# Kernel tuning notes

Hardware: AMD Instinct MI355X
Metric: run time of the kernel (lower is better)

## Reference

```python
import jax, jax.numpy as jnp
import numpy as np

IN_DIM = 128
SLOT_SIZE = 64
NUM_SLOTS = 8
NUM_ITERS = 3
MLP_HDIM = 128
EPSILON = 1e-08


def _layernorm(x, g, b, eps=1e-5):
    m = jnp.mean(x, axis=-1, keepdims=True)
    v = jnp.mean((x - m) ** 2, axis=-1, keepdims=True)
    return (x - m) * jax.lax.rsqrt(v + eps) * g + b


def setup_inputs() -> dict:
    key = jax.random.key(0)
    ks = jax.random.split(key, 16)
    H, D, K, M = SLOT_SIZE, IN_DIM, NUM_SLOTS, MLP_HDIM
    x = jax.random.normal(ks[0], (32, 4096, D), dtype=jnp.float32)
    noise = jax.random.normal(ks[1], (32, K, H), dtype=jnp.float32)
    s = lambda k, shape, fan_in: jax.random.normal(k, shape, jnp.float32) * (1.0 / np.sqrt(fan_in))
    return {
        'x': x,
        'noise': noise,
        'Wq': s(ks[2], (H, H), H),            # project_q (no bias)
        'Wk': s(ks[3], (H, D), D),            # project_k
        'Wv': s(ks[4], (H, D), D),            # project_v
        'ln_in_g': jnp.ones((D,), jnp.float32), 'ln_in_b': jnp.zeros((D,), jnp.float32),
        'ln_sl_g': jnp.ones((H,), jnp.float32), 'ln_sl_b': jnp.zeros((H,), jnp.float32),
        'ln_mlp_g': jnp.ones((H,), jnp.float32), 'ln_mlp_b': jnp.zeros((H,), jnp.float32),
        'gru_w_ih': s(ks[5], (3 * H, H), H),  # PyTorch GRUCell weight_ih (r,z,n)
        'gru_w_hh': s(ks[6], (3 * H, H), H),
        'gru_b_ih': jnp.zeros((3 * H,), jnp.float32),
        'gru_b_hh': jnp.zeros((3 * H,), jnp.float32),
        'mlp_w1': s(ks[7], (M, H), H), 'mlp_b1': jnp.zeros((M,), jnp.float32),
        'mlp_w2': s(ks[8], (H, M), M), 'mlp_b2': jnp.zeros((H,), jnp.float32),
        'slots_mu': jnp.tile(jnp.linspace(-1.0, 1.0, K, dtype=jnp.float32)[None, :, None], (1, 1, H)),
        'slots_logsigma': jnp.full((1, K, H), -1.0, dtype=jnp.float32),
    }


def reference(x, noise, Wq, Wk, Wv, ln_in_g, ln_in_b, ln_sl_g, ln_sl_b,
              ln_mlp_g, ln_mlp_b, gru_w_ih, gru_w_hh, gru_b_ih, gru_b_hh,
              mlp_w1, mlp_b1, mlp_w2, mlp_b2, slots_mu, slots_logsigma):
    B = x.shape[0]
    H, K = SLOT_SIZE, NUM_SLOTS
    xn = _layernorm(x, ln_in_g, ln_in_b)
    k = jnp.einsum('bnd,hd->bnh', xn, Wk)  # [B,N,H]
    v = jnp.einsum('bnd,hd->bnh', xn, Wv)

    scale = jax.nn.softplus(slots_logsigma) + 1e-05
    slots = slots_mu + scale * noise  # rsample, broadcast over batch -> [B,K,H]

    def step(slots):
        slots_prev = slots
        s = _layernorm(slots, ln_sl_g, ln_sl_b)
        q = jnp.einsum('bkh,gh->bkg', s, Wq)  # [B,K,H]
        scores = (H ** -0.5) * jnp.einsum('bnh,bkh->bnk', k, q)
        attn = jax.nn.softmax(scores, axis=-1) + EPSILON  # softmax over slots
        attn = attn / jnp.sum(attn, axis=1, keepdims=True)  # normalize over inputs
        updates = jnp.einsum('bnk,bnh->bkh', attn, v)
        # PyTorch GRUCell: gates ordered (r, z, n)
        u = updates.reshape(-1, H)
        h = slots_prev.reshape(-1, H)
        gx = u @ gru_w_ih.T + gru_b_ih
        gh = h @ gru_w_hh.T + gru_b_hh
        xr, xz, xn_ = jnp.split(gx, 3, axis=-1)
        hr, hz, hn = jnp.split(gh, 3, axis=-1)
        r = jax.nn.sigmoid(xr + hr)
        z = jax.nn.sigmoid(xz + hz)
        n = jnp.tanh(xn_ + r * hn)
        slots = ((1.0 - z) * n + z * h).reshape(B, K, H)
        slots = _layernorm(slots, ln_mlp_g, ln_mlp_b)
        mlp_out = jax.nn.relu(slots @ mlp_w1.T + mlp_b1) @ mlp_w2.T + mlp_b2
        return slots + mlp_out

    for _ in range(NUM_ITERS):
        slots = step(slots)
    return slots
```

## Files before the change

### kernel.cpp

```cpp
#include <hip/hip_runtime.h>

typedef __attribute__((ext_vector_type(8))) short s16x8;
typedef __attribute__((ext_vector_type(4))) float f32x4;

#define DEV static __device__ __forceinline__

DEV float b2f(unsigned short u){
  unsigned int i = ((unsigned int)u) << 16;
  float f; __builtin_memcpy(&f, &i, 4); return f;
}
DEV unsigned short f2b(float f){
  unsigned int i; __builtin_memcpy(&i, &f, 4);
  i = i + 0x7fffu + ((i >> 16) & 1u);
  return (unsigned short)(i >> 16);
}
DEV f32x4 mfma16(s16x8 a, s16x8 b, f32x4 c){
  return __builtin_amdgcn_mfma_f32_16x16x32_bf16(a, b, c, 0, 0, 0);
}
DEV s16x8 ld8f(const float* p){
  const float4* q4 = (const float4*)p;
  float4 a = q4[0], b = q4[1];
  s16x8 r;
  r[0]=(short)f2b(a.x); r[1]=(short)f2b(a.y); r[2]=(short)f2b(a.z); r[3]=(short)f2b(a.w);
  r[4]=(short)f2b(b.x); r[5]=(short)f2b(b.y); r[6]=(short)f2b(b.z); r[7]=(short)f2b(b.w);
  return r;
}

template<int C> DEV float dpp_addstep(float x){
  int y = __builtin_amdgcn_update_dpp(0, __builtin_bit_cast(int, x), C, 0xF, 0xF, true);
  return x + __builtin_bit_cast(float, y);
}
DEV float rsum16(float v){
  v = dpp_addstep<0xB1>(v);
  v = dpp_addstep<0x4E>(v);
  v = dpp_addstep<0x141>(v);
  v = dpp_addstep<0x140>(v);
  return v;
}

__global__ __launch_bounds__(256) void k_wpack(
    const float* __restrict__ Wk, const float* __restrict__ Wv,
    const float* __restrict__ wih, const float* __restrict__ whh,
    const float* __restrict__ w1, const float* __restrict__ w2,
    const float* __restrict__ Wq,
    unsigned short* __restrict__ wkb, unsigned short* __restrict__ wvb,
    unsigned short* __restrict__ wall)
{
  int t = blockIdx.x * 256 + threadIdx.x;
  int off = t * 4;
  const float* src; unsigned short* dst;
  if      (off <  8192){ src = Wk  + off;         dst = wkb  + off; }
  else if (off < 16384){ src = Wv  + off -  8192; dst = wvb  + off - 8192; }
  else if (off < 28672){ src = wih + off - 16384; dst = wall + off - 16384; }
  else if (off < 40960){ src = whh + off - 28672; dst = wall + off - 16384; }
  else if (off < 49152){ src = w1  + off - 40960; dst = wall + off - 16384; }
  else if (off < 57344){ src = w2  + off - 49152; dst = wall + off - 16384; }
  else                 { src = Wq  + off - 57344; dst = wall + off - 16384; }
  float4 v = *(const float4*)src;
  ushort4 o;
  o.x = f2b(v.x); o.y = f2b(v.y); o.z = f2b(v.z); o.w = f2b(v.w);
  *(ushort4*)dst = o;
}

__global__ __launch_bounds__(256, 4) void k_lnkv7(
    const float* __restrict__ x,
    const unsigned short* __restrict__ wkb,
    const unsigned short* __restrict__ wvb,
    const float* __restrict__ lg,
    const float* __restrict__ lb,
    unsigned short* __restrict__ kg,
    unsigned short* __restrict__ vt,
    const float* __restrict__ noise,
    const float* __restrict__ mu,
    const float* __restrict__ lsg,
    const float* __restrict__ gsl,
    const float* __restrict__ bsl,
    const float* __restrict__ Wq,
    float* __restrict__ slots,
    unsigned short* __restrict__ qws)
{
  __shared__ __align__(16) unsigned int xs[128 * 68];
  const int tid = threadIdx.x;
  const int w = tid >> 6, ln = tid & 63;
  const int m16 = ln & 15, q = ln >> 4;

  if (blockIdx.x >= 1024){
    unsigned short* st = (unsigned short*)xs;
    float (*redS)[4] = (float(*)[4])((char*)xs + 2304);
    float (*redQ)[4] = (float(*)[4])((char*)xs + 2560);
    const int bi = blockIdx.x - 1024;
    const int r0 = bi * 16;
    const int cw = w*16 + m16;

    float sl[4], s1[4], s2[4];
    #pragma unroll
    for (int rr = 0; rr < 4; ++rr){
      int row = r0 + q*4 + rr;
      int k = row & 7;
      float v = mu[k*64 + cw] + (log1pf(expf(lsg[k*64 + cw])) + 1e-5f) * noise[row*64 + cw];
      sl[rr] = v;
      slots[row*64 + cw] = v;
      s1[rr] = rsum16(v);
      s2[rr] = rsum16(v*v);
    }
    if (m16 == 0){
      #pragma unroll
      for (int rr = 0; rr < 4; ++rr){ redS[q*4+rr][w] = s1[rr]; redQ[q*4+rr][w] = s2[rr]; }
    }
    __syncthreads();
    {
      const float gs = gsl[cw], bs = bsl[cw];
      #pragma unroll
      for (int rr = 0; rr < 4; ++rr){
        f32x4 aS = *(const f32x4*)redS[q*4+rr];
        f32x4 aQ = *(const f32x4*)redQ[q*4+rr];
        float tS = aS[0]+aS[1]+aS[2]+aS[3];
        float tQ = aQ[0]+aQ[1]+aQ[2]+aQ[3];
        float mean = tS*(1.f/64.f);
        float var  = tQ*(1.f/64.f) - mean*mean;
        float rs = rsqrtf(var + 1e-5f);
        float sq = (sl[rr] - mean)*rs*gs + bs;
        st[(q*4+rr)*72 + cw] = f2b(sq);
      }
    }
    __syncthreads();
    {
      f32x4 acc = {0,0,0,0};
      #pragma unroll
      for (int ks = 0; ks < 2; ++ks){
        s16x8 a = *(const s16x8*)(st + m16*72 + ks*32 + q*8);
        acc = mfma16(a, ld8f(Wq + cw*64 + ks*32 + q*8), acc);
      }
      #pragma unroll
      for (int rr = 0; rr < 4; ++rr){
        int row = r0 + q*4 + rr;
        int bb_ = row >> 3, kk = row & 7;
        qws[(bb_*16 + kk)*64 + cw] = f2b(acc[rr] * 0.125f);
      }
      int b0 = bi * 2;
      ((unsigned int*)(qws + (b0*16 + 8)*64))[tid] = 0u;
      ((unsigned int*)(qws + ((b0+1)*16 + 8)*64))[tid] = 0u;
    }
    return;
  }

  const int b = blockIdx.x >> 5;
  const int nbase = (blockIdx.x & 31) << 7;
  const long rowg0 = (long)b * 4096 + nbase;

  {
    const int c = m16;
    const float4 gA = *(const float4*)(lg + c*4);
    const float4 gB = *(const float4*)(lg + 64 + c*4);
    const float4 bA = *(const float4*)(lb + c*4);
    const float4 bB = *(const float4*)(lb + 64 + c*4);
    const float* base = x + (rowg0 + w*32 + q)*128;

    float4 va[4], vb[4];
    #pragma unroll
    for (int i = 0; i < 3; ++i){
      va[i] = *(const float4*)(base + i*512 + c*4);
      vb[i] = *(const float4*)(base + i*512 + 64 + c*4);
    }
    #pragma unroll
    for (int p = 0; p < 8; ++p){
      const int cur = p & 3;
      if (p < 5){
        const int nxt = (p+3) & 3;
        va[nxt] = *(const float4*)(base + (p+3)*512 + c*4);
        vb[nxt] = *(const float4*)(base + (p+3)*512 + 64 + c*4);
      }
      float4 u = va[cur], t = vb[cur];
      float s1 = (u.x + u.y) + (u.z + u.w) + (t.x + t.y) + (t.z + t.w);
      float s2 = (u.x*u.x + u.y*u.y) + (u.z*u.z + u.w*u.w)
               + (t.x*t.x + t.y*t.y) + (t.z*t.z + t.w*t.w);
      s1 = rsum16(s1);
      s2 = rsum16(s2);
      float mean = s1 * (1.f/128.f);
      float var  = s2 * (1.f/128.f) - mean*mean;
      float rs = rsqrtf(var + 1e-5f);
      float y0 = (u.x - mean)*rs*gA.x + bA.x;
      float y1 = (u.y - mean)*rs*gA.y + bA.y;
      float y2 = (u.z - mean)*rs*gA.z + bA.z;
      float y3 = (u.w - mean)*rs*gA.w + bA.w;
      float y4 = (t.x - mean)*rs*gB.x + bB.x;
      float y5 = (t.y - mean)*rs*gB.y + bB.y;
      float y6 = (t.z - mean)*rs*gB.z + bB.z;
      float y7 = (t.w - mean)*rs*gB.w + bB.w;
      uint2 pkA, pkB;
      pkA.x = (unsigned int)f2b(y0) | ((unsigned int)f2b(y1) << 16);
      pkA.y = (unsigned int)f2b(y2) | ((unsigned int)f2b(y3) << 16);
      pkB.x = (unsigned int)f2b(y4) | ((unsigned int)f2b(y5) << 16);
      pkB.y = (unsigned int)f2b(y6) | ((unsigned int)f2b(y7) << 16);
      const int r = w*32 + p*4 + q;
      *(uint2*)&xs[r*68 + c*2] = pkA;
      *(uint2*)&xs[r*68 + 32 + c*2] = pkB;
    }
  }

  s16x8 bw[4][4];
  #pragma unroll
  for (int t = 0; t < 4; ++t)
    #pragma unroll
    for (int kb = 0; kb < 4; ++kb)
      bw[kb][t] = *(const s16x8*)(wkb + (t*16 + m16)*128 + kb*32 + q*8);

  __syncthreads();

  const f32x4 zf = {0.f, 0.f, 0.f, 0.f};

  #pragma unroll
  for (int mi = 0; mi < 2; ++mi){
    int n0 = (w*2 + mi) * 16;
    f32x4 acc[4];
    #pragma unroll
    for (int t = 0; t < 4; ++t) acc[t] = zf;
    #pragma unroll
    for (int kb = 0; kb < 4; ++kb){
      s16x8 af = *(const s16x8*)((const unsigned short*)(xs + (n0 + m16)*68) + kb*32 + q*8);
      #pragma unroll
      for (int t = 0; t < 4; ++t)
        acc[t] = mfma16(af, bw[kb][t], acc[t]);
    }
    #pragma unroll
    for (int t = 0; t < 4; ++t){
      int h = t*16 + m16;
      #pragma unroll
      for (int rr = 0; rr < 4; ++rr){
        long n = rowg0 + n0 + q*4 + rr;
        kg[n*64 + h] = f2b(acc[t][rr]);
      }
    }
  }

  #pragma unroll
  for (int t = 0; t < 4; ++t)
    #pragma unroll
    for (int kb = 0; kb < 4; ++kb)
      bw[kb][t] = *(const s16x8*)(wvb + (t*16 + m16)*128 + kb*32 + q*8);

  #pragma unroll
  for (int mi = 0; mi < 2; ++mi){
    int n0 = (w*2 + mi) * 16;
    f32x4 acc[4];
    #pragma unroll
    for (int t = 0; t < 4; ++t) acc[t] = zf;
    #pragma unroll
    for (int kb = 0; kb < 4; ++kb){
      s16x8 af = *(const s16x8*)((const unsigned short*)(xs + (n0 + m16)*68) + kb*32 + q*8);
      #pragma unroll
      for (int t = 0; t < 4; ++t)
        acc[t] = mfma16(af, bw[kb][t], acc[t]);
    }
    #pragma unroll
    for (int t = 0; t < 4; ++t){
      int h = t*16 + m16;
      unsigned int p0 = (unsigned int)f2b(acc[t][0]) | ((unsigned int)f2b(acc[t][1]) << 16);
      unsigned int p1 = (unsigned int)f2b(acc[t][2]) | ((unsigned int)f2b(acc[t][3]) << 16);
      uint2 pv; pv.x = p0; pv.y = p1;
      long off = ((long)b*64 + h)*4096 + nbase + n0 + q*4;
      *(uint2*)(vt + off) = pv;
    }
  }
}

__global__ __launch_bounds__(256) void k_attn3(
    const unsigned short* __restrict__ kg,
    const unsigned short* __restrict__ vt,
    const unsigned short* __restrict__ qws,
    const unsigned short* __restrict__ wall,
    const float* __restrict__ bih, const float* __restrict__ bhh,
    const float* __restrict__ b1p, const float* __restrict__ b2p,
    const float* __restrict__ gmlp, const float* __restrict__ bmlp,
    const float* __restrict__ gsl, const float* __restrict__ bsl,
    const float* __restrict__ Up_in, const float* __restrict__ Sp_in,
    float* __restrict__ Up_out, float* __restrict__ Sp_out,
    const float* __restrict__ slin, float* __restrict__ slout,
    int it)
{
  __shared__ float sc[256*17];
  __shared__ unsigned short aT[16*264];
  __shared__ unsigned short ut[16*72], ht[16*72], st[16*72], hid[16*136];
  __shared__ unsigned short qloc[16*72];
  __shared__ __align__(16) float redS[16][4];
  __shared__ __align__(16) float redQ[16][4];
  __shared__ __align__(16) float redS2[16][4];
  __shared__ __align__(16) float redQ2[16][4];

  const int tid = threadIdx.x;
  const int w = tid >> 6, ln = tid & 63;
  const int m16 = ln & 15, q = ln >> 4;

  const int p_   = blockIdx.x;
  const int xcd  = p_ & 7;
  const int slot = p_ >> 3;
  const int lb   = ((xcd << 1) + (slot >> 5))*32 + (slot & 31);
  const int b = lb >> 4;
  const int tile = lb & 15;
  const int nbase = tile << 8;

  s16x8 afp[4];
  #pragma unroll
  for (int mi = 0; mi < 4; ++mi){
    int n0 = (w*4 + mi)*16;
    afp[mi] = *(const s16x8*)(kg + ((long)b*4096 + nbase + n0 + m16)*64 + q*8);
  }
  s16x8 afp2[4];
  #pragma unroll
  for (int mi = 0; mi < 4; ++mi){
    int n0 = (w*4 + mi)*16;
    afp2[mi] = *(const s16x8*)(kg + ((long)b*4096 + nbase + n0 + m16)*64 + 32 + q*8);
  }
  s16x8 vtp[8];
  #pragma unroll
  for (int ks = 0; ks < 8; ++ks)
    vtp[ks] = *(const s16x8*)(vt + ((long)b*64 + w*16 + m16)*4096 + nbase + ks*32 + q*8);

  for (int i = tid; i < 8*264; i += 256) aT[8*264 + i] = 0;
  if (tid < 128){
    int row = 8 + (tid >> 4), c = (tid & 15)*4;
    ushort4 z4 = {0,0,0,0};
    *(ushort4*)&qloc[row*72 + c] = z4;
  }

  if (it == 0){
    if (tid < 128){
      int row = tid >> 4, c = (tid & 15)*4;
      *(ushort4*)&qloc[row*72 + c] = *(const ushort4*)(qws + (b*16 + row)*64 + c);
    }
  } else {
    const int r0 = (b >> 1) * 16;
    const int cw = w*16 + m16;
    const unsigned short* wihb = wall;
    const unsigned short* whhb = wall + 12288;
    const unsigned short* w1b  = wall + 24576;
    const unsigned short* w2b  = wall + 32768;
    const unsigned short* wqb  = wall + 40960;

    #pragma unroll
    for (int p = 0; p < 4; ++p){
      int row = p*4 + w;
      int g = r0 + row;
      int bb = g >> 3, sl = g & 7;
      const float* up  = Up_in + ((bb*16)*8 + sl)*64 + ln;
      const float* spp = Sp_in + (bb*16)*8 + sl;
      float usum = 0.f, ssum = 0.f;
      #pragma unroll
      for (int t = 0; t < 16; ++t){
        usum += up[t*512];
        ssum += spp[t*8];
      }
      ut[row*72 + ln] = f2b(usum / ssum);
      ht[row*72 + ln] = f2b(slin[g*64 + ln]);
    }
    __syncthreads();

    f32x4 axr = {0,0,0,0}, axz = {0,0,0,0}, axn = {0,0,0,0};
    f32x4 ahr = {0,0,0,0}, ahz = {0,0,0,0}, ahn = {0,0,0,0};
    #pragma unroll
    for (int ks = 0; ks < 2; ++ks){
      s16x8 au = *(const s16x8*)(ut + m16*72 + ks*32 + q*8);
      s16x8 ah = *(const s16x8*)(ht + m16*72 + ks*32 + q*8);
      axr = mfma16(au, *(const s16x8*)(wihb + (      cw)*64 + ks*32 + q*8), axr);
      axz = mfma16(au, *(const s16x8*)(wihb + ( 64 + cw)*64 + ks*32 + q*8), axz);
      axn = mfma16(au, *(const s16x8*)(wihb + (128 + cw)*64 + ks*32 + q*8), axn);
      ahr = mfma16(ah, *(const s16x8*)(whhb + (      cw)*64 + ks*32 + q*8), ahr);
      ahz = mfma16(ah, *(const s16x8*)(whhb + ( 64 + cw)*64 + ks*32 + q*8), ahz);
      ahn = mfma16(ah, *(const s16x8*)(whhb + (128 + cw)*64 + ks*32 + q*8), ahn);
    }
    const float bxr = bih[cw], bxz = bih[64+cw], bxn = bih[128+cw];
    const float bhr = bhh[cw], bhz = bhh[64+cw], bhn = bhh[128+cw];
    float sp[4];
    #pragma unroll
    for (int rr = 0; rr < 4; ++rr){
      float xr = axr[rr] + bxr, xz = axz[rr] + bxz, xnv = axn[rr] + bxn;
      float hr = ahr[rr] + bhr, hz = ahz[rr] + bhz, hn = ahn[rr] + bhn;
      float rg = 1.f / (1.f + expf(-(xr + hr)));
      float zg = 1.f / (1.f + expf(-(xz + hz)));
      float ng = tanhf(xnv + rg*hn);
      float hv = b2f(ht[(q*4 + rr)*72 + cw]);
      sp[rr] = (1.f - zg)*ng + zg*hv;
    }

    float s1[4], s2[4];
    #pragma unroll
    for (int rr = 0; rr < 4; ++rr){
      s1[rr] = rsum16(sp[rr]);
      s2[rr] = rsum16(sp[rr]*sp[rr]);
    }
    if (m16 == 0){
      #pragma unroll
      for (int rr = 0; rr < 4; ++rr){ redS[q*4+rr][w] = s1[rr]; redQ[q*4+rr][w] = s2[rr]; }
    }
    __syncthreads();
    float sl_[4];
    {
      const float gm = gmlp[cw], bm = bmlp[cw];
      #pragma unroll
      for (int rr = 0; rr < 4; ++rr){
        f32x4 aS = *(const f32x4*)redS[q*4+rr];
        f32x4 aQ = *(const f32x4*)redQ[q*4+rr];
        float tS = aS[0]+aS[1]+aS[2]+aS[3];
        float tQ = aQ[0]+aQ[1]+aQ[2]+aQ[3];
        float mean = tS*(1.f/64.f);
        float var  = tQ*(1.f/64.f) - mean*mean;
        float rs = rsqrtf(var + 1e-5f);
        sl_[rr] = (sp[rr] - mean)*rs*gm + bm;
        st[(q*4+rr)*72 + cw] = f2b(sl_[rr]);
      }
    }
    __syncthreads();

    #pragma unroll
    for (int t2 = 0; t2 < 2; ++t2){
      int nt = w*2 + t2;
      int col = nt*16 + m16;
      f32x4 acc = {0,0,0,0};
      #pragma unroll
      for (int ks = 0; ks < 2; ++ks){
        s16x8 a = *(const s16x8*)(st + m16*72 + ks*32 + q*8);
        acc = mfma16(a, *(const s16x8*)(w1b + col*64 + ks*32 + q*8), acc);
      }
      float bb = b1p[col];
      #pragma unroll
      for (int rr = 0; rr < 4; ++rr)
        hid[(q*4+rr)*136 + col] = f2b(fmaxf(acc[rr] + bb, 0.f));
    }
    __syncthreads();

    float snew[4];
    {
      f32x4 acc = {0,0,0,0};
      #pragma unroll
      for (int ks = 0; ks < 4; ++ks){
        s16x8 a = *(const s16x8*)(hid + m16*136 + ks*32 + q*8);
        acc = mfma16(a, *(const s16x8*)(w2b + cw*128 + ks*32 + q*8), acc);
      }
      float bb = b2p[cw];
      #pragma unroll
      for (int rr = 0; rr < 4; ++rr){
        snew[rr] = sl_[rr] + acc[rr] + bb;
        if ((lb & 31) == 0)
          slout[(r0 + q*4 + rr)*64 + cw] = snew[rr];
      }
    }

    #pragma unroll
    for (int rr = 0; rr < 4; ++rr){
      s1[rr] = rsum16(snew[rr]);
      s2[rr] = rsum16(snew[rr]*snew[rr]);
    }
    if (m16 == 0){
      #pragma unroll
      for (int rr = 0; rr < 4; ++rr){ redS2[q*4+rr][w] = s1[rr]; redQ2[q*4+rr][w] = s2[rr]; }
    }
    __syncthreads();
    {
      const float gs = gsl[cw], bs = bsl[cw];
      #pragma unroll
      for (int rr = 0; rr < 4; ++rr){
        f32x4 aS = *(const f32x4*)redS2[q*4+rr];
        f32x4 aQ = *(const f32x4*)redQ2[q*4+rr];
        float tS = aS[0]+aS[1]+aS[2]+aS[3];
        float tQ = aQ[0]+aQ[1]+aQ[2]+aQ[3];
        float mean = tS*(1.f/64.f);
        float var  = tQ*(1.f/64.f) - mean*mean;
        float rs = rsqrtf(var + 1e-5f);
        float sq = (snew[rr] - mean)*rs*gs + bs;
        st[(q*4+rr)*72 + cw] = f2b(sq);
      }
    }
    __syncthreads();
    {
      f32x4 acc = {0,0,0,0};
      #pragma unroll
      for (int ks = 0; ks < 2; ++ks){
        s16x8 a = *(const s16x8*)(st + m16*72 + ks*32 + q*8);
        acc = mfma16(a, *(const s16x8*)(wqb + cw*64 + ks*32 + q*8), acc);
      }
      #pragma unroll
      for (int rr = 0; rr < 4; ++rr){
        int rloc = q*4 + rr;
        if ((rloc >> 3) == (b & 1))
          qloc[(rloc & 7)*72 + cw] = f2b(acc[rr] * 0.125f);
      }
    }
  }
  __syncthreads();

  s16x8 bq[2];
  #pragma unroll
  for (int ks = 0; ks < 2; ++ks)
    bq[ks] = *(const s16x8*)(qloc + m16*72 + ks*32 + q*8);

  #pragma unroll
  for (int mi = 0; mi < 4; ++mi){
    int n0 = (w*4 + mi)*16;
    f32x4 acc = {0.f, 0.f, 0.f, 0.f};
    acc = mfma16(afp[mi],  bq[0], acc);
    acc = mfma16(afp2[mi], bq[1], acc);
    #pragma unroll
    for (int rr = 0; rr < 4; ++rr)
      sc[(n0 + q*4 + rr)*17 + m16] = acc[rr];
  }
  __syncthreads();

  {
    int r = tid;
    float a8[8];
    float mx = -1e30f;
    #pragma unroll
    for (int j = 0; j < 8; ++j){ a8[j] = sc[r*17 + j]; mx = fmaxf(mx, a8[j]); }
    float ssum = 0.f;
    #pragma unroll
    for (int j = 0; j < 8; ++j){ a8[j] = expf(a8[j] - mx); ssum += a8[j]; }
    float inv = 1.f/ssum;
    #pragma unroll
    for (int j = 0; j < 8; ++j)
      aT[j*264 + r] = f2b(a8[j]*inv + 1e-8f);
  }
  __syncthreads();

  {
    int j = tid >> 5, c = tid & 31;
    float p = 0.f;
    #pragma unroll
    for (int i = 0; i < 8; ++i) p += b2f(aT[j*264 + c + 32*i]);
    p = rsum16(p);
    p += __shfl_xor(p, 16);
    if ((tid & 31) == 0) Sp_out[(b*16 + tile)*8 + j] = p;
  }

  {
    f32x4 acc = {0.f, 0.f, 0.f, 0.f};
    #pragma unroll
    for (int ks = 0; ks < 8; ++ks){
      s16x8 af = *(const s16x8*)(aT + m16*264 + ks*32 + q*8);
      acc = mfma16(af, vtp[ks], acc);
    }
    float* ub = Up_out + ((b*16 + tile)*8)*64 + w*16 + m16;
    #pragma unroll
    for (int rr = 0; rr < 4; ++rr){
      int slot2 = q*4 + rr;
      if (slot2 < 8)
        ub[slot2*64] = acc[rr];
    }
  }
}

__global__ __launch_bounds__(256) void k_gru2(
    const float* __restrict__ Up, const float* __restrict__ Sp,
    const float* __restrict__ slots,
    const float* __restrict__ wih, const float* __restrict__ whh,
    const float* __restrict__ bih, const float* __restrict__ bhh,
    const float* __restrict__ w1, const float* __restrict__ b1p,
    const float* __restrict__ w2, const float* __restrict__ b2p,
    const float* __restrict__ gmlp, const float* __restrict__ bmlp,
    float* __restrict__ outp)
{
  __shared__ unsigned short ut[16*72], ht[16*72], st[16*72], hid[16*136];
  __shared__ __align__(16) float redS[16][4];
  __shared__ __align__(16) float redQ[16][4];
  const int tid = threadIdx.x;
  const int w = tid >> 6, ln = tid & 63;
  const int m16 = ln & 15, q = ln >> 4;
  const int r0 = blockIdx.x * 16;
  const int cw = w*16 + m16;

  #pragma unroll
  for (int p = 0; p < 4; ++p){
    int row = p*4 + w;
    int g = r0 + row;
    int bb = g >> 3, sl = g & 7;
    const float* up  = Up + ((bb*16)*8 + sl)*64 + ln;
    const float* spp = Sp + (bb*16)*8 + sl;
    float usum = 0.f, ssum = 0.f;
    #pragma unroll
    for (int t = 0; t < 16; ++t){
      usum += up[t*512];
      ssum += spp[t*8];
    }
    ut[row*72 + ln] = f2b(usum / ssum);
    ht[row*72 + ln] = f2b(slots[g*64 + ln]);
  }
  __syncthreads();

  f32x4 axr = {0,0,0,0}, axz = {0,0,0,0}, axn = {0,0,0,0};
  f32x4 ahr = {0,0,0,0}, ahz = {0,0,0,0}, ahn = {0,0,0,0};
  #pragma unroll
  for (int ks = 0; ks < 2; ++ks){
    s16x8 au = *(const s16x8*)(ut + m16*72 + ks*32 + q*8);
    s16x8 ah = *(const s16x8*)(ht + m16*72 + ks*32 + q*8);
    axr = mfma16(au, ld8f(wih + (      cw)*64 + ks*32 + q*8), axr);
    axz = mfma16(au, ld8f(wih + ( 64 + cw)*64 + ks*32 + q*8), axz);
    axn = mfma16(au, ld8f(wih + (128 + cw)*64 + ks*32 + q*8), axn);
    ahr = mfma16(ah, ld8f(whh + (      cw)*64 + ks*32 + q*8), ahr);
    ahz = mfma16(ah, ld8f(whh + ( 64 + cw)*64 + ks*32 + q*8), ahz);
    ahn = mfma16(ah, ld8f(whh + (128 + cw)*64 + ks*32 + q*8), ahn);
  }
  const float bxr = bih[cw], bxz = bih[64+cw], bxn = bih[128+cw];
  const float bhr = bhh[cw], bhz = bhh[64+cw], bhn = bhh[128+cw];
  float sp[4];
  #pragma unroll
  for (int rr = 0; rr < 4; ++rr){
    float xr = axr[rr] + bxr, xz = axz[rr] + bxz, xnv = axn[rr] + bxn;
    float hr = ahr[rr] + bhr, hz = ahz[rr] + bhz, hn = ahn[rr] + bhn;
    float rg = 1.f / (1.f + expf(-(xr + hr)));
    float zg = 1.f / (1.f + expf(-(xz + hz)));
    float ng = tanhf(xnv + rg*hn);
    float hv = b2f(ht[(q*4 + rr)*72 + cw]);
    sp[rr] = (1.f - zg)*ng + zg*hv;
  }

  float s1[4], s2[4];
  #pragma unroll
  for (int rr = 0; rr < 4; ++rr){
    s1[rr] = rsum16(sp[rr]);
    s2[rr] = rsum16(sp[rr]*sp[rr]);
  }
  if (m16 == 0){
    #pragma unroll
    for (int rr = 0; rr < 4; ++rr){ redS[q*4+rr][w] = s1[rr]; redQ[q*4+rr][w] = s2[rr]; }
  }
  __syncthreads();
  float sl_[4];
  {
    const float gm = gmlp[cw], bm = bmlp[cw];
    #pragma unroll
    for (int rr = 0; rr < 4; ++rr){
      f32x4 aS = *(const f32x4*)redS[q*4+rr];
      f32x4 aQ = *(const f32x4*)redQ[q*4+rr];
      float tS = aS[0]+aS[1]+aS[2]+aS[3];
      float tQ = aQ[0]+aQ[1]+aQ[2]+aQ[3];
      float mean = tS*(1.f/64.f);
      float var  = tQ*(1.f/64.f) - mean*mean;
      float rs = rsqrtf(var + 1e-5f);
      sl_[rr] = (sp[rr] - mean)*rs*gm + bm;
      st[(q*4+rr)*72 + cw] = f2b(sl_[rr]);
    }
  }
  __syncthreads();

  #pragma unroll
  for (int t2 = 0; t2 < 2; ++t2){
    int nt = w*2 + t2;
    int col = nt*16 + m16;
    f32x4 acc = {0,0,0,0};
    #pragma unroll
    for (int ks = 0; ks < 2; ++ks){
      s16x8 a = *(const s16x8*)(st + m16*72 + ks*32 + q*8);
      acc = mfma16(a, ld8f(w1 + col*64 + ks*32 + q*8), acc);
    }
    float bb = b1p[col];
    #pragma unroll
    for (int rr = 0; rr < 4; ++rr)
      hid[(q*4+rr)*136 + col] = f2b(fmaxf(acc[rr] + bb, 0.f));
  }
  __syncthreads();

  {
    f32x4 acc = {0,0,0,0};
    #pragma unroll
    for (int ks = 0; ks < 4; ++ks){
      s16x8 a = *(const s16x8*)(hid + m16*136 + ks*32 + q*8);
      acc = mfma16(a, ld8f(w2 + cw*128 + ks*32 + q*8), acc);
    }
    float bb = b2p[cw];
    #pragma unroll
    for (int rr = 0; rr < 4; ++rr){
      int row = r0 + q*4 + rr;
      outp[row*64 + cw] = sl_[rr] + acc[rr] + bb;
    }
  }
}

extern "C" void kernel_launch(void* const* d_in, const int* in_sizes, int n_in,
                              void* d_out, int out_size, void* d_ws, size_t ws_size,
                              hipStream_t stream)
{
  const float* x    = (const float*)d_in[0];
  const float* noise= (const float*)d_in[1];
  const float* Wq   = (const float*)d_in[2];
  const float* Wk   = (const float*)d_in[3];
  const float* Wv   = (const float*)d_in[4];
  const float* ling = (const float*)d_in[5];
  const float* linb = (const float*)d_in[6];
  const float* gsl  = (const float*)d_in[7];
  const float* bsl  = (const float*)d_in[8];
  const float* gmlp = (const float*)d_in[9];
  const float* bmlp = (const float*)d_in[10];
  const float* wih  = (const float*)d_in[11];
  const float* whh  = (const float*)d_in[12];
  const float* bih  = (const float*)d_in[13];
  const float* bhh  = (const float*)d_in[14];
  const float* w1   = (const float*)d_in[15];
  const float* b1p  = (const float*)d_in[16];
  const float* w2   = (const float*)d_in[17];
  const float* b2p  = (const float*)d_in[18];
  const float* mu   = (const float*)d_in[19];
  const float* lsg  = (const float*)d_in[20];

  char* ws = (char*)d_ws;
  unsigned short* kg   = (unsigned short*)(ws);
  unsigned short* vt   = (unsigned short*)(ws + 16777216);
  char* base = ws + 33554432;
  unsigned short* qws  = (unsigned short*)(base);
  float* slotsA        = (float*)(base + 65536);
  float* slotsB        = (float*)(base + 131072);
  float* slotsC        = (float*)(base + 196608);
  float* UA            = (float*)(base + 262144);
  float* UB            = (float*)(base + 1310720);
  float* SA            = (float*)(base + 2359296);
  float* SB            = (float*)(base + 2375680);
  unsigned short* wkb  = (unsigned short*)(base + 2392064);
  unsigned short* wvb  = (unsigned short*)(base + 2408448);
  unsigned short* wall = (unsigned short*)(base + 2424832);
  float* outp          = (float*)d_out;

  hipLaunchKernelGGL(k_wpack, dim3(60), dim3(256), 0, stream,
                     Wk, Wv, wih, whh, w1, w2, Wq, wkb, wvb, wall);
  hipLaunchKernelGGL(k_lnkv7, dim3(1040), dim3(256), 0, stream,
                     x, wkb, wvb, ling, linb, kg, vt,
                     noise, mu, lsg, gsl, bsl, Wq, slotsA, qws);
  hipLaunchKernelGGL(k_attn3, dim3(512), dim3(256), 0, stream,
                     kg, vt, qws, wall, bih, bhh, b1p, b2p, gmlp, bmlp, gsl, bsl,
                     UA, SA, UA, SA, slotsA, slotsA, 0);
  hipLaunchKernelGGL(k_attn3, dim3(512), dim3(256), 0, stream,
                     kg, vt, qws, wall, bih, bhh, b1p, b2p, gmlp, bmlp, gsl, bsl,
                     UA, SA, UB, SB, slotsA, slotsB, 1);
  hipLaunchKernelGGL(k_attn3, dim3(512), dim3(256), 0, stream,
                     kg, vt, qws, wall, bih, bhh, b1p, b2p, gmlp, bmlp, gsl, bsl,
                     UB, SB, UA, SA, slotsB, slotsC, 2);
  hipLaunchKernelGGL(k_gru2, dim3(16), dim3(256), 0, stream, UA, SA, slotsC,
                     wih, whh, bih, bhh, w1, b1p, w2, b2p, gmlp, bmlp, outp);
  (void)in_sizes; (void)n_in; (void)out_size; (void)ws_size;
}
```

Measured before the change: 199.3 us.

## Fuse first attention iteration into LN/KV projection kernel via precomputed q·Wk

Initial slot sampling, LayerNorm and q projection move into the weight-pack kernel, which also precomputes q·Wk so that first-iteration scores can be taken directly from normalized x. The LN/KV kernel then computes first-iteration softmax, attention sums and partial updates while x is still in shared memory. This removes one full attention launch and its re-read of k and v. In exchange the LN/KV kernel does more work per block, uses more registers, and the next attention kernel has to reduce 32 partials per batch instead of 16.

```diff
diff --git a/kernel.cpp b/kernel.cpp
--- a/kernel.cpp
+++ b/kernel.cpp
@@ -30,6 +30,10 @@
   int y = __builtin_amdgcn_update_dpp(0, __builtin_bit_cast(int, x), C, 0xF, 0xF, true);
   return x + __builtin_bit_cast(float, y);
 }
+template<int C> DEV float dpp_maxstep(float x){
+  int y = __builtin_amdgcn_update_dpp(0, __builtin_bit_cast(int, x), C, 0xF, 0xF, true);
+  return fmaxf(x, __builtin_bit_cast(float, y));
+}
 DEV float rsum16(float v){
   v = dpp_addstep<0xB1>(v);
   v = dpp_addstep<0x4E>(v);
@@ -37,32 +41,142 @@
   v = dpp_addstep<0x140>(v);
   return v;
 }
-
-__global__ __launch_bounds__(256) void k_wpack(
+DEV float rmax16(float v){
+  v = dpp_maxstep<0xB1>(v);
+  v = dpp_maxstep<0x4E>(v);
+  v = dpp_maxstep<0x141>(v);
+  v = dpp_maxstep<0x140>(v);
+  return v;
+}
+
+__global__ __launch_bounds__(256) void k_wpack2(
     const float* __restrict__ Wk, const float* __restrict__ Wv,
     const float* __restrict__ wih, const float* __restrict__ whh,
     const float* __restrict__ w1, const float* __restrict__ w2,
     const float* __restrict__ Wq,
     unsigned short* __restrict__ wkb, unsigned short* __restrict__ wvb,
-    unsigned short* __restrict__ wall)
+    unsigned short* __restrict__ wall,
+    const float* __restrict__ noise,
+    const float* __restrict__ mu,
+    const float* __restrict__ lsg,
+    const float* __restrict__ gsl,
+    const float* __restrict__ bsl,
+    float* __restrict__ slots,
+    unsigned short* __restrict__ qws,
+    unsigned short* __restrict__ qk2g)
 {
-  int t = blockIdx.x * 256 + threadIdx.x;
-  int off = t * 4;
-  const float* src; unsigned short* dst;
-  if      (off <  8192){ src = Wk  + off;         dst = wkb  + off; }
-  else if (off < 16384){ src = Wv  + off -  8192; dst = wvb  + off - 8192; }
-  else if (off < 28672){ src = wih + off - 16384; dst = wall + off - 16384; }
-  else if (off < 40960){ src = whh + off - 28672; dst = wall + off - 16384; }
-  else if (off < 49152){ src = w1  + off - 40960; dst = wall + off - 16384; }
-  else if (off < 57344){ src = w2  + off - 49152; dst = wall + off - 16384; }
-  else                 { src = Wq  + off - 57344; dst = wall + off - 16384; }
-  float4 v = *(const float4*)src;
-  ushort4 o;
-  o.x = f2b(v.x); o.y = f2b(v.y); o.z = f2b(v.z); o.w = f2b(v.w);
-  *(ushort4*)dst = o;
-}
-
-__global__ __launch_bounds__(256, 4) void k_lnkv7(
+  const int tid = threadIdx.x;
+  if (blockIdx.x < 60){
+    int t = blockIdx.x * 256 + tid;
+    int off = t * 4;
+    const float* src; unsigned short* dst;
+    if      (off <  8192){ src = Wk  + off;         dst = wkb  + off; }
+    else if (off < 16384){ src = Wv  + off -  8192; dst = wvb  + off - 8192; }
+    else if (off < 28672){ src = wih + off - 16384; dst = wall + off - 16384; }
+    else if (off < 40960){ src = whh + off - 28672; dst = wall + off - 16384; }
+    else if (off < 49152){ src = w1  + off - 40960; dst = wall + off - 16384; }
+    else if (off < 57344){ src = w2  + off - 49152; dst = wall + off - 16384; }
+    else                 { src = Wq  + off - 57344; dst = wall + off - 16384; }
+    float4 v = *(const float4*)src;
+    ushort4 o;
+    o.x = f2b(v.x); o.y = f2b(v.y); o.z = f2b(v.z); o.w = f2b(v.w);
+    *(ushort4*)dst = o;
+    return;
+  }
+
+  __shared__ unsigned short st[16*72];
+  __shared__ unsigned short wkl[8192];
+  __shared__ __align__(16) float redS[16][4];
+  __shared__ __align__(16) float redQ[16][4];
+  const int w = tid >> 6, ln = tid & 63;
+  const int m16 = ln & 15, q = ln >> 4;
+  const int bi = blockIdx.x - 60;
+  const int r0 = bi * 16;
+  const int cw = w*16 + m16;
+
+  for (int i = tid; i < 2048; i += 256){
+    float4 v = ((const float4*)Wk)[i];
+    ushort4 o;
+    o.x = f2b(v.x); o.y = f2b(v.y); o.z = f2b(v.z); o.w = f2b(v.w);
+    ((ushort4*)wkl)[i] = o;
+  }
+
+  float sl[4], s1[4], s2[4];
+  #pragma unroll
+  for (int rr = 0; rr < 4; ++rr){
+    int row = r0 + q*4 + rr;
+    int k = row & 7;
+    float v = mu[k*64 + cw] + (log1pf(expf(lsg[k*64 + cw])) + 1e-5f) * noise[row*64 + cw];
+    sl[rr] = v;
+    slots[row*64 + cw] = v;
+    s1[rr] = rsum16(v);
+    s2[rr] = rsum16(v*v);
+  }
+  if (m16 == 0){
+    #pragma unroll
+    for (int rr = 0; rr < 4; ++rr){ redS[q*4+rr][w] = s1[rr]; redQ[q*4+rr][w] = s2[rr]; }
+  }
+  __syncthreads();
+  {
+    const float gs = gsl[cw], bs = bsl[cw];
+    #pragma unroll
+    for (int rr = 0; rr < 4; ++rr){
+      f32x4 aS = *(const f32x4*)redS[q*4+rr];
+      f32x4 aQ = *(const f32x4*)redQ[q*4+rr];
+      float tS = aS[0]+aS[1]+aS[2]+aS[3];
+      float tQ = aQ[0]+aQ[1]+aQ[2]+aQ[3];
+      float mean = tS*(1.f/64.f);
+      float var  = tQ*(1.f/64.f) - mean*mean;
+      float rs = rsqrtf(var + 1e-5f);
+      float sq = (sl[rr] - mean)*rs*gs + bs;
+      st[(q*4+rr)*72 + cw] = f2b(sq);
+    }
+  }
+  __syncthreads();
+  unsigned short qv[4];
+  {
+    f32x4 acc = {0,0,0,0};
+    #pragma unroll
+    for (int ks = 0; ks < 2; ++ks){
+      s16x8 a = *(const s16x8*)(st + m16*72 + ks*32 + q*8);
+      acc = mfma16(a, ld8f(Wq + cw*64 + ks*32 + q*8), acc);
+    }
+    #pragma unroll
+    for (int rr = 0; rr < 4; ++rr){
+      int row = r0 + q*4 + rr;
+      int bb_ = row >> 3, kk = row & 7;
+      qv[rr] = f2b(acc[rr] * 0.125f);
+      qws[(bb_*16 + kk)*64 + cw] = qv[rr];
+    }
+    int b0 = bi * 2;
+    ((unsigned int*)(qws + (b0*16 + 8)*64))[tid] = 0u;
+    ((unsigned int*)(qws + ((b0+1)*16 + 8)*64))[tid] = 0u;
+  }
+  __syncthreads();
+  #pragma unroll
+  for (int rr = 0; rr < 4; ++rr)
+    st[(q*4+rr)*72 + cw] = qv[rr];
+  __syncthreads();
+
+  for (int idx = tid; idx < 2048; idx += 256){
+    int lb2  = idx >> 10;
+    int rem  = idx & 1023;
+    int slot = rem >> 7;
+    int d    = rem & 127;
+    int srow = lb2*8 + slot;
+    float s = 0.f;
+    #pragma unroll
+    for (int h = 0; h < 64; ++h)
+      s += b2f(st[srow*72 + h]) * b2f(wkl[h*128 + d]);
+    qk2g[(((bi*2 + lb2)*16) + slot)*128 + d] = f2b(s);
+  }
+  for (int i = tid; i < 512; i += 256){
+    ((unsigned int*)(qk2g + ((bi*2    )*16 + 8)*128))[i] = 0u;
+    ((unsigned int*)(qk2g + ((bi*2 + 1)*16 + 8)*128))[i] = 0u;
+  }
+}
+
+__global__ __launch_bounds__(256, 4) void k_lnkv8(
     const float* __restrict__ x,
     const unsigned short* __restrict__ wkb,
     const unsigned short* __restrict__ wvb,
@@ -70,82 +184,17 @@
     const float* __restrict__ lb,
     unsigned short* __restrict__ kg,
     unsigned short* __restrict__ vt,
-    const float* __restrict__ noise,
-    const float* __restrict__ mu,
-    const float* __restrict__ lsg,
-    const float* __restrict__ gsl,
-    const float* __restrict__ bsl,
-    const float* __restrict__ Wq,
-    float* __restrict__ slots,
-    unsigned short* __restrict__ qws)
+    const unsigned short* __restrict__ qk2g,
+    float* __restrict__ Up0, float* __restrict__ Sp0)
 {
   __shared__ __align__(16) unsigned int xs[128 * 68];
   const int tid = threadIdx.x;
   const int w = tid >> 6, ln = tid & 63;
   const int m16 = ln & 15, q = ln >> 4;
 
-  if (blockIdx.x >= 1024){
-    unsigned short* st = (unsigned short*)xs;
-    float (*redS)[4] = (float(*)[4])((char*)xs + 2304);
-    float (*redQ)[4] = (float(*)[4])((char*)xs + 2560);
-    const int bi = blockIdx.x - 1024;
-    const int r0 = bi * 16;
-    const int cw = w*16 + m16;
-
-    float sl[4], s1[4], s2[4];
-    #pragma unroll
-    for (int rr = 0; rr < 4; ++rr){
-      int row = r0 + q*4 + rr;
-      int k = row & 7;
-      float v = mu[k*64 + cw] + (log1pf(expf(lsg[k*64 + cw])) + 1e-5f) * noise[row*64 + cw];
-      sl[rr] = v;
-      slots[row*64 + cw] = v;
-      s1[rr] = rsum16(v);
-      s2[rr] = rsum16(v*v);
-    }
-    if (m16 == 0){
-      #pragma unroll
-      for (int rr = 0; rr < 4; ++rr){ redS[q*4+rr][w] = s1[rr]; redQ[q*4+rr][w] = s2[rr]; }
-    }
-    __syncthreads();
-    {
-      const float gs = gsl[cw], bs = bsl[cw];
-      #pragma unroll
-      for (int rr = 0; rr < 4; ++rr){
-        f32x4 aS = *(const f32x4*)redS[q*4+rr];
-        f32x4 aQ = *(const f32x4*)redQ[q*4+rr];
-        float tS = aS[0]+aS[1]+aS[2]+aS[3];
-        float tQ = aQ[0]+aQ[1]+aQ[2]+aQ[3];
-        float mean = tS*(1.f/64.f);
-        float var  = tQ*(1.f/64.f) - mean*mean;
-        float rs = rsqrtf(var + 1e-5f);
-        float sq = (sl[rr] - mean)*rs*gs + bs;
-        st[(q*4+rr)*72 + cw] = f2b(sq);
-      }
-    }
-    __syncthreads();
-    {
-      f32x4 acc = {0,0,0,0};
-      #pragma unroll
-      for (int ks = 0; ks < 2; ++ks){
-        s16x8 a = *(const s16x8*)(st + m16*72 + ks*32 + q*8);
-        acc = mfma16(a, ld8f(Wq + cw*64 + ks*32 + q*8), acc);
-      }
-      #pragma unroll
-      for (int rr = 0; rr < 4; ++rr){
-        int row = r0 + q*4 + rr;
-        int bb_ = row >> 3, kk = row & 7;
-        qws[(bb_*16 + kk)*64 + cw] = f2b(acc[rr] * 0.125f);
-      }
-      int b0 = bi * 2;
-      ((unsigned int*)(qws + (b0*16 + 8)*64))[tid] = 0u;
-      ((unsigned int*)(qws + ((b0+1)*16 + 8)*64))[tid] = 0u;
-    }
-    return;
-  }
-
   const int b = blockIdx.x >> 5;
-  const int nbase = (blockIdx.x & 31) << 7;
+  const int t128 = blockIdx.x & 31;
+  const int nbase = t128 << 7;
   const long rowg0 = (long)b * 4096 + nbase;
 
   {
@@ -239,35 +288,120 @@
     for (int kb = 0; kb < 4; ++kb)
       bw[kb][t] = *(const s16x8*)(wvb + (t*16 + m16)*128 + kb*32 + q*8);
 
+  f32x4 accV[2][4];
   #pragma unroll
   for (int mi = 0; mi < 2; ++mi){
+    #pragma unroll
+    for (int t = 0; t < 4; ++t) accV[mi][t] = zf;
+    #pragma unroll
+    for (int kb = 0; kb < 4; ++kb){
+      int n0 = (w*2 + mi) * 16;
+      s16x8 af = *(const s16x8*)((const unsigned short*)(xs + (n0 + m16)*68) + kb*32 + q*8);
+      #pragma unroll
+      for (int t = 0; t < 4; ++t)
+        accV[mi][t] = mfma16(af, bw[kb][t], accV[mi][t]);
+    }
     int n0 = (w*2 + mi) * 16;
-    f32x4 acc[4];
-    #pragma unroll
-    for (int t = 0; t < 4; ++t) acc[t] = zf;
-    #pragma unroll
-    for (int kb = 0; kb < 4; ++kb){
-      s16x8 af = *(const s16x8*)((const unsigned short*)(xs + (n0 + m16)*68) + kb*32 + q*8);
-      #pragma unroll
-      for (int t = 0; t < 4; ++t)
-        acc[t] = mfma16(af, bw[kb][t], acc[t]);
-    }
     #pragma unroll
     for (int t = 0; t < 4; ++t){
       int h = t*16 + m16;
-      unsigned int p0 = (unsigned int)f2b(acc[t][0]) | ((unsigned int)f2b(acc[t][1]) << 16);
-      unsigned int p1 = (unsigned int)f2b(acc[t][2]) | ((unsigned int)f2b(acc[t][3]) << 16);
+      unsigned int p0 = (unsigned int)f2b(accV[mi][t][0]) | ((unsigned int)f2b(accV[mi][t][1]) << 16);
+      unsigned int p1 = (unsigned int)f2b(accV[mi][t][2]) | ((unsigned int)f2b(accV[mi][t][3]) << 16);
       uint2 pv; pv.x = p0; pv.y = p1;
       long off = ((long)b*64 + h)*4096 + nbase + n0 + q*4;
       *(uint2*)(vt + off) = pv;
     }
   }
+
+  s16x8 bqk[4];
+  #pragma unroll
+  for (int kb = 0; kb < 4; ++kb)
+    bqk[kb] = *(const s16x8*)(qk2g + ((long)b*16 + m16)*128 + kb*32 + q*8);
+
+  f32x4 accS[2];
+  #pragma unroll
+  for (int mi = 0; mi < 2; ++mi){
+    accS[mi] = zf;
+    int n0 = (w*2 + mi) * 16;
+    #pragma unroll
+    for (int kb = 0; kb < 4; ++kb){
+      s16x8 af = *(const s16x8*)((const unsigned short*)(xs + (n0 + m16)*68) + kb*32 + q*8);
+      accS[mi] = mfma16(af, bqk[kb], accS[mi]);
+    }
+  }
+  __syncthreads();
+
+  unsigned short* vtile = (unsigned short*)xs;
+  unsigned short* aTl   = (unsigned short*)xs + 8704;
+  float (*redPS)[4]     = (float(*)[4])((char*)xs + 21760);
+
+  for (int i = tid; i < 1088; i += 256) ((unsigned int*)aTl)[i] = 0u;
+  __syncthreads();
+
+  #pragma unroll
+  for (int mi = 0; mi < 2; ++mi){
+    int n0 = (w*2 + mi) * 16;
+    #pragma unroll
+    for (int t = 0; t < 4; ++t){
+      unsigned int p0 = (unsigned int)f2b(accV[mi][t][0]) | ((unsigned int)f2b(accV[mi][t][1]) << 16);
+      unsigned int p1 = (unsigned int)f2b(accV[mi][t][2]) | ((unsigned int)f2b(accV[mi][t][3]) << 16);
+      uint2 pv; pv.x = p0; pv.y = p1;
+      *(uint2*)(vtile + (t*16 + m16)*136 + n0 + q*4) = pv;
+    }
+  }
+
+  float s_loc = 0.f;
+  #pragma unroll
+  for (int mi = 0; mi < 2; ++mi){
+    int n0 = (w*2 + mi) * 16;
+    unsigned short av[4];
+    #pragma unroll
+    for (int rr = 0; rr < 4; ++rr){
+      float vm = (m16 < 8) ? accS[mi][rr] : -1e30f;
+      float mx = rmax16(vm);
+      float e  = (m16 < 8) ? expf(accS[mi][rr] - mx) : 0.f;
+      float ss = rsum16(e);
+      float a  = e * (1.f/ss) + 1e-8f;
+      av[rr] = f2b(a);
+      if (m16 < 8) s_loc += b2f(av[rr]);
+    }
+    if (m16 < 8){
+      unsigned int p0 = (unsigned int)av[0] | ((unsigned int)av[1] << 16);
+      unsigned int p1 = (unsigned int)av[2] | ((unsigned int)av[3] << 16);
+      uint2 pv; pv.x = p0; pv.y = p1;
+      *(uint2*)(aTl + m16*136 + n0 + q*4) = pv;
+    }
+  }
+  s_loc += __shfl_xor(s_loc, 16);
+  s_loc += __shfl_xor(s_loc, 32);
+  if (q == 0 && m16 < 8) redPS[m16][w] = s_loc;
+  __syncthreads();
+  if (tid < 8){
+    f32x4 r = *(const f32x4*)redPS[tid];
+    Sp0[((long)b*32 + t128)*8 + tid] = r[0]+r[1]+r[2]+r[3];
+  }
+
+  {
+    f32x4 accU = zf;
+    #pragma unroll
+    for (int ks = 0; ks < 4; ++ks){
+      s16x8 afA = *(const s16x8*)(aTl + m16*136 + ks*32 + q*8);
+      s16x8 bfV = *(const s16x8*)(vtile + (w*16 + m16)*136 + ks*32 + q*8);
+      accU = mfma16(afA, bfV, accU);
+    }
+    float* ub = Up0 + (((long)b*32 + t128)*8)*64 + w*16 + m16;
+    #pragma unroll
+    for (int rr = 0; rr < 4; ++rr){
+      int slot = q*4 + rr;
+      if (slot < 8)
+        ub[slot*64] = accU[rr];
+    }
+  }
 }
 
 __global__ __launch_bounds__(256) void k_attn3(
     const unsigned short* __restrict__ kg,
     const unsigned short* __restrict__ vt,
-    const unsigned short* __restrict__ qws,
     const unsigned short* __restrict__ wall,
     const float* __restrict__ bih, const float* __restrict__ bhh,
     const float* __restrict__ b1p, const float* __restrict__ b2p,
@@ -276,7 +410,7 @@
     const float* __restrict__ Up_in, const float* __restrict__ Sp_in,
     float* __restrict__ Up_out, float* __restrict__ Sp_out,
     const float* __restrict__ slin, float* __restrict__ slout,
-    int it)
+    int npart)
 {
   __shared__ float sc[256*17];
   __shared__ unsigned short aT[16*264];
@@ -299,16 +433,11 @@
   const int tile = lb & 15;
   const int nbase = tile << 8;
 
-  s16x8 afp[4];
+  s16x8 afp[4], afp2[4];
   #pragma unroll
   for (int mi = 0; mi < 4; ++mi){
     int n0 = (w*4 + mi)*16;
-    afp[mi] = *(const s16x8*)(kg + ((long)b*4096 + nbase + n0 + m16)*64 + q*8);
-  }
-  s16x8 afp2[4];
-  #pragma unroll
-  for (int mi = 0; mi < 4; ++mi){
-    int n0 = (w*4 + mi)*16;
+    afp[mi]  = *(const s16x8*)(kg + ((long)b*4096 + nbase + n0 + m16)*64 + q*8);
     afp2[mi] = *(const s16x8*)(kg + ((long)b*4096 + nbase + n0 + m16)*64 + 32 + q*8);
   }
   s16x8 vtp[8];
@@ -323,12 +452,7 @@
     *(ushort4*)&qloc[row*72 + c] = z4;
   }
 
-  if (it == 0){
-    if (tid < 128){
-      int row = tid >> 4, c = (tid & 15)*4;
-      *(ushort4*)&qloc[row*72 + c] = *(const ushort4*)(qws + (b*16 + row)*64 + c);
-    }
-  } else {
+  {
     const int r0 = (b >> 1) * 16;
     const int cw = w*16 + m16;
     const unsigned short* wihb = wall;
@@ -342,13 +466,15 @@
       int row = p*4 + w;
       int g = r0 + row;
       int bb = g >> 3, sl = g & 7;
-      const float* up  = Up_in + ((bb*16)*8 + sl)*64 + ln;
-      const float* spp = Sp_in + (bb*16)*8 + sl;
+      const float* up  = Up_in + ((long)(bb*npart)*8 + sl)*64 + ln;
+      const float* spp = Sp_in + (long)(bb*npart)*8 + sl;
       float usum = 0.f, ssum = 0.f;
-      #pragma unroll
-      for (int t = 0; t < 16; ++t){
-        usum += up[t*512];
-        ssum += spp[t*8];
+      if (npart == 32){
+        #pragma unroll
+        for (int t = 0; t < 32; ++t){ usum += up[t*512]; ssum += spp[t*8]; }
+      } else {
+        #pragma unroll
+        for (int t = 0; t < 16; ++t){ usum += up[t*512]; ssum += spp[t*8]; }
       }
       ut[row*72 + ln] = f2b(usum / ssum);
       ht[row*72 + ln] = f2b(slin[g*64 + ln]);
@@ -528,7 +654,7 @@
     for (int i = 0; i < 8; ++i) p += b2f(aT[j*264 + c + 32*i]);
     p = rsum16(p);
     p += __shfl_xor(p, 16);
-    if ((tid & 31) == 0) Sp_out[(b*16 + tile)*8 + j] = p;
+    if ((tid & 31) == 0) Sp_out[((long)b*16 + tile)*8 + j] = p;
   }
 
   {
@@ -538,7 +664,7 @@
       s16x8 af = *(const s16x8*)(aT + m16*264 + ks*32 + q*8);
       acc = mfma16(af, vtp[ks], acc);
     }
-    float* ub = Up_out + ((b*16 + tile)*8)*64 + w*16 + m16;
+    float* ub = Up_out + (((long)b*16 + tile)*8)*64 + w*16 + m16;
     #pragma unroll
     for (int rr = 0; rr < 4; ++rr){
       int slot2 = q*4 + rr;
@@ -708,30 +834,30 @@
   float* slotsA        = (float*)(base + 65536);
   float* slotsB        = (float*)(base + 131072);
   float* slotsC        = (float*)(base + 196608);
-  float* UA            = (float*)(base + 262144);
-  float* UB            = (float*)(base + 1310720);
-  float* SA            = (float*)(base + 2359296);
-  float* SB            = (float*)(base + 2375680);
-  unsigned short* wkb  = (unsigned short*)(base + 2392064);
-  unsigned short* wvb  = (unsigned short*)(base + 2408448);
-  unsigned short* wall = (unsigned short*)(base + 2424832);
+  float* Up0           = (float*)(base + 262144);
+  float* U1            = (float*)(base + 2359296);
+  float* U2            = (float*)(base + 3407872);
+  float* Sp0           = (float*)(base + 4456448);
+  float* S1            = (float*)(base + 4489216);
+  float* S2            = (float*)(base + 4505600);
+  unsigned short* wkb  = (unsigned short*)(base + 4521984);
+  unsigned short* wvb  = (unsigned short*)(base + 4538368);
+  unsigned short* wall = (unsigned short*)(base + 4554752);
+  unsigned short* qk2g = (unsigned short*)(base + 4644864);
   float* outp          = (float*)d_out;
 
-  hipLaunchKernelGGL(k_wpack, dim3(60), dim3(256), 0, stream,
-                     Wk, Wv, wih, whh, w1, w2, Wq, wkb, wvb, wall);
-  hipLaunchKernelGGL(k_lnkv7, dim3(1040), dim3(256), 0, stream,
-                     x, wkb, wvb, ling, linb, kg, vt,
-                     noise, mu, lsg, gsl, bsl, Wq, slotsA, qws);
+  hipLaunchKernelGGL(k_wpack2, dim3(76), dim3(256), 0, stream,
+                     Wk, Wv, wih, whh, w1, w2, Wq, wkb, wvb, wall,
+                     noise, mu, lsg, gsl, bsl, slotsA, qws, qk2g);
+  hipLaunchKernelGGL(k_lnkv8, dim3(1024), dim3(256), 0, stream,
+                     x, wkb, wvb, ling, linb, kg, vt, qk2g, Up0, Sp0);
   hipLaunchKernelGGL(k_attn3, dim3(512), dim3(256), 0, stream,
-                     kg, vt, qws, wall, bih, bhh, b1p, b2p, gmlp, bmlp, gsl, bsl,
-                     UA, SA, UA, SA, slotsA, slotsA, 0);
+                     kg, vt, wall, bih, bhh, b1p, b2p, gmlp, bmlp, gsl, bsl,
+                     Up0, Sp0, U1, S1, slotsA, slotsB, 32);
   hipLaunchKernelGGL(k_attn3, dim3(512), dim3(256), 0, stream,
-                     kg, vt, qws, wall, bih, bhh, b1p, b2p, gmlp, bmlp, gsl, bsl,
-                     UA, SA, UB, SB, slotsA, slotsB, 1);
-  hipLaunchKernelGGL(k_attn3, dim3(512), dim3(256), 0, stream,
-                     kg, vt, qws, wall, bih, bhh, b1p, b2p, gmlp, bmlp, gsl, bsl,
-                     UB, SB, UA, SA, slotsB, slotsC, 2);
-  hipLaunchKernelGGL(k_gru2, dim3(16), dim3(256), 0, stream, UA, SA, slotsC,
+                     kg, vt, wall, bih, bhh, b1p, b2p, gmlp, bmlp, gsl, bsl,
+                     U1, S1, U2, S2, slotsB, slotsC, 16);
+  hipLaunchKernelGGL(k_gru2, dim3(16), dim3(256), 0, stream, U2, S2, slotsC,
                      wih, whh, bih, bhh, w1, b1p, w2, b2p, gmlp, bmlp, outp);
   (void)in_sizes; (void)n_in; (void)out_size; (void)ws_size;
 }
```

New measurement: 212.3 us. +6.5%, slower.
